# Kernel tuning notes

Hardware: AMD Instinct MI355X
Metric: run time of the kernel (lower is better)

## Reference

```python
import jax, jax.numpy as jnp
import numpy as np

SR = 44100
LOWEST_HZ = 55.0
N_FRAMES = 100
L_ORDER = 5                       # l_filter_order
NC = L_ORDER + 1                  # num_coefficients
NA = L_ORDER + 2                  # num_active_indexes
V = int(SR // LOWEST_HZ) + NA     # coeff_vector_size = 808
N_SAMPLES = 44100


def _nat_cubic_spline_eval(y, t_out):
    """Natural cubic spline through y (n_knots, d) on uniform knots in [0,1],
    evaluated at t_out (T,). Returns (T, d)."""
    n, d = y.shape
    h = 1.0 / (n - 1)
    # second derivatives M: natural BC -> M[0] = M[n-1] = 0, tridiagonal solve
    rhs = 6.0 * (y[2:] - 2.0 * y[1:-1] + y[:-2]) / h        # (n-2, d)
    T = (jnp.diag(jnp.full((n - 2,), 4.0 * h))
         + jnp.diag(jnp.full((n - 3,), h), 1)
         + jnp.diag(jnp.full((n - 3,), h), -1))
    M_in = jnp.linalg.solve(T, rhs)
    M = jnp.concatenate([jnp.zeros((1, d), y.dtype), M_in, jnp.zeros((1, d), y.dtype)])
    idx = jnp.clip((t_out / h).astype(jnp.int32), 0, n - 2)
    f = (t_out - idx.astype(y.dtype) * h)[:, None]          # fractional offset
    y0, y1 = y[idx], y[idx + 1]
    M0, M1 = M[idx], M[idx + 1]
    bcoef = (y1 - y0) / h - h * (2.0 * M0 + M1) / 6.0
    ccoef = 0.5 * M0
    dcoef = (M1 - M0) / (6.0 * h)
    return y0 + f * (bcoef + f * (ccoef + f * dcoef))


def _sample_wise_lpc(x, a):
    """Time-varying all-pole filter: y[t] = x[t] - sum_i a[t, i] * y[t-1-i].
    x: (T,), a: (T, p) -> y: (T,)."""
    p = a.shape[1]

    def step(hist, inp):
        xt, at = inp
        yt = xt - jnp.dot(at, hist)
        hist = jnp.concatenate([yt[None], hist[:-1]])
        return hist, yt

    _, y = jax.lax.scan(step, jnp.zeros((p,), x.dtype), (x, a))
    return y


def setup_inputs() -> dict:
    key = jax.random.key(0)
    k1, k2, k3, k4 = jax.random.split(key, 4)
    # delay in samples, ~[300, 500] -> f0 in [88, 147] Hz, safely inside V=808
    delay_len_frames = 300.0 + 200.0 * jax.random.uniform(k1, (N_FRAMES,), dtype=jnp.float32)
    raw_gain = jnp.full((1,), 2.5, jnp.float32)             # sigmoid -> ~0.924 loop gain
    # raw coeffs uniform in (-2, 0) like the torch init
    raw_coeff_frames = -2.0 * jax.random.uniform(k2, (N_FRAMES, NC), dtype=jnp.float32)
    excitation = jax.random.normal(k3, (N_SAMPLES,), dtype=jnp.float32)
    exc_coefficients = 0.01 * jax.random.normal(k4, (1, N_SAMPLES, 1), dtype=jnp.float32)
    return {"delay_len_frames": delay_len_frames, "raw_gain": raw_gain,
            "raw_coeff_frames": raw_coeff_frames, "excitation": excitation,
            "exc_coefficients": exc_coefficients, "n_samples": N_SAMPLES}


def reference(delay_len_frames, raw_gain, raw_coeff_frames, excitation,
              exc_coefficients, n_samples):
    # constrained, normalized loop-filter coefficients per frame
    gain = jax.nn.sigmoid(raw_gain)                          # (1,)
    sig = jax.nn.sigmoid(raw_coeff_frames)                   # (F, NC)
    b_frames = sig / jnp.sum(sig, -1, keepdims=True) * gain

    # upsample delay + coeffs jointly with one natural cubic spline
    params = jnp.concatenate([delay_len_frames[:, None], b_frames], axis=1)  # (F, NC+1)
    t_out = jnp.linspace(0.0, 1.0, n_samples)
    up = _nat_cubic_spline_eval(params, t_out)               # (T, NC+1)
    delay, b = up[:, 0], up[:, 1:]

    z = jnp.floor(delay).astype(jnp.int32)                   # integer delay
    alfa = delay - jnp.floor(delay)                          # fractional part

    # scatter-build the per-sample sparse filter rows into dense A (T, V)
    cols = z[:, None] + jnp.arange(NA)[None, :]              # (T, NA)
    first = (-(1.0 - alfa) * b[:, 0])[:, None]
    mid = -(alfa[:, None] * b[:, :-1] + (1.0 - alfa)[:, None] * b[:, 1:])
    last = (-alfa * b[:, -1])[:, None]
    vals = jnp.concatenate([first, mid, last], axis=1)       # (T, NA)
    A = jnp.zeros((n_samples, V), jnp.float32).at[
        jnp.arange(n_samples)[:, None], cols].set(vals)

    # excitation shaping (order-1 time-varying all-pole), then KS string loop
    x = _sample_wise_lpc(excitation, exc_coefficients[0])
    y = _sample_wise_lpc(x, A)
    return y
```

## Files before the change

kernel.cpp:

```cpp
#include <hip/hip_runtime.h>

#define NSMP 44100
#define NKNOT 100
#define NIV  (NKNOT - 1)
#define NCC 6
#define NAA 7
#define RING 1024
#define NTH 320
#define SEG ((NSMP + NTH - 1) / NTH)
#define GW 8
#define NHEAT 256
#define HEAT_SLEEPS 6

__device__ __forceinline__ float sigm(float x) { return 1.0f / (1.0f + expf(-x)); }

__device__ __forceinline__ void lean_barrier() {
    asm volatile("s_waitcnt lgkmcnt(0)" ::: "memory");
    __builtin_amdgcn_s_barrier();
    __builtin_amdgcn_sched_barrier(0);
}

__device__ __forceinline__ void compute_rec(const float4 (*CO)[8], int t, bool a,
                                            float* wr, int* raOut) {
    const float H   = 1.0f / 99.0f;
    const float INV = 1.0f / (float)(NSMP - 1);
    if (!a) {
#pragma unroll
        for (int d = 0; d < NAA; ++d) wr[d] = 0.0f;
        *raOut = 0;
        return;
    }
    float tt = (float)t * INV;
    int idx = (int)(tt * 99.0f); if (idx > NIV - 1) idx = NIV - 1;
    float f = tt - (float)idx * H;
    float r[NAA];
#pragma unroll
    for (int c = 0; c < NAA; ++c) {
        float4 k = CO[idx][c];
        r[c] = k.x + f * (k.y + f * (k.z + f * k.w));
    }
    float fl = floorf(r[0]);
    float alfa = r[0] - fl, om = 1.0f - alfa;
    wr[6] = -om * r[1];
    wr[5] = -(alfa * r[1] + om * r[2]);
    wr[4] = -(alfa * r[2] + om * r[3]);
    wr[3] = -(alfa * r[3] + om * r[4]);
    wr[2] = -(alfa * r[4] + om * r[5]);
    wr[1] = -(alfa * r[5] + om * r[6]);
    wr[0] = -alfa * r[6];
    *raOut = (t - 1 - (int)fl - 6) & (RING - 1);
}

__global__ __launch_bounds__(NTH, 1) void diffks_kernel(
    const float* __restrict__ dlf, const float* __restrict__ rg,
    const float* __restrict__ rcf, const float* __restrict__ exc,
    const float* __restrict__ ecoef, float* __restrict__ out,
    float* __restrict__ ws, int ws_ok)
{
    if (blockIdx.x != 0) {
        float v = 1.0f + 0.125f * (float)(blockIdx.x & 7);
#pragma unroll 1
        for (int k = 0; k < HEAT_SLEEPS; ++k) {
            __builtin_amdgcn_s_sleep(127);
            v = fmaf(v, 1.000001f, 1.0e-6f);
        }
        asm volatile("" :: "v"(v));
        if (ws_ok && threadIdx.x == 0) ws[blockIdx.x] = v;
        return;
    }

    __shared__ float  P[NKNOT][NAA];
    __shared__ float  M[NKNOT][NAA];
    __shared__ float4 CO[NIV][8];
    __shared__ float  ring[2 * RING];
    __shared__ float  CPs[NKNOT - 2];
    __shared__ float  IMs[NKNOT - 2];
    __shared__ float  wpS[NTH / 64], wqS[NTH / 64];
    __shared__ int    s_minz;

    const int tid  = threadIdx.x;
    const int lane = tid & 63;
    const int wav  = tid >> 6;
    const float H   = 1.0f / 99.0f;

    if (tid == 0) s_minz = 0x7fffffff;
    for (int i = tid; i < 2 * RING; i += NTH) ring[i] = 0.0f;

    if (tid < NKNOT) {
        float g = sigm(rg[0]);
        float s[NCC];
        float sum = 0.0f;
#pragma unroll
        for (int j = 0; j < NCC; ++j) { s[j] = sigm(rcf[tid * NCC + j]); sum += s[j]; }
        P[tid][0] = dlf[tid];
#pragma unroll
        for (int j = 0; j < NCC; ++j) P[tid][j + 1] = s[j] / sum * g;
    }
    if (tid < NKNOT - 2) {
        float cp = 0.25f;
        int n = tid; if (n > 10) n = 10;
        for (int k = 0; k < n; ++k) cp = 1.0f / (4.0f - cp);
        CPs[tid] = cp;
    }
    __syncthreads();
    if (tid >= 1 && tid < NKNOT - 2) IMs[tid] = 99.0f / (4.0f - CPs[tid - 1]);
    __syncthreads();

    if (tid < NAA) {
        int c = tid;
        float rhs0  = 6.0f * (P[2][c] - 2.0f * P[1][c] + P[0][c]) * 99.0f;
        float dprev = rhs0 * 24.75f;
        M[1][c] = dprev;
        for (int i = 1; i < NKNOT - 2; ++i) {
            float rhs = 6.0f * (P[i + 2][c] - 2.0f * P[i + 1][c] + P[i][c]) * 99.0f;
            float d   = (rhs - H * dprev) * IMs[i];
            M[i + 1][c] = d;
            dprev = d;
        }
        float nxt = M[NKNOT - 2][c];
        for (int i = NKNOT - 4; i >= 0; --i) {
            float v = M[i + 1][c] - CPs[i] * nxt;
            M[i + 1][c] = v;
            nxt = v;
        }
        M[0][c] = 0.0f;
        M[NKNOT - 1][c] = 0.0f;
    }
    __syncthreads();

    if (tid < NIV) {
        float lb = fminf(P[tid][0], P[tid + 1][0])
                 - (H * H * 0.125f) * fmaxf(fabsf(M[tid][0]), fabsf(M[tid + 1][0]));
        atomicMin(&s_minz, (int)floorf(lb));
    }

    for (int iv = tid; iv < NIV; iv += NTH) {
#pragma unroll
        for (int c = 0; c < NAA; ++c) {
            float y0 = P[iv][c], y1 = P[iv + 1][c];
            float m0 = M[iv][c], m1 = M[iv + 1][c];
            float b  = (y1 - y0) * 99.0f - H * (2.0f * m0 + m1) * (1.0f / 6.0f);
            CO[iv][c] = make_float4(y0, b, 0.5f * m0, (m1 - m0) * (99.0f / 6.0f));
        }
    }
    __syncthreads();

    {
        int start = tid * SEG;
        int end   = min(start + SEG, NSMP);
        float p = 1.0f, q = 0.0f;
#pragma unroll 4
        for (int t = start; t < end; ++t) {
            float a2 = ecoef[t];
            q = fmaf(-a2, q, exc[t]);
            p *= -a2;
        }
#pragma unroll
        for (int d = 1; d < 64; d <<= 1) {
            float pp = __shfl_up(p, d);
            float qq = __shfl_up(q, d);
            if (lane >= d) { q = fmaf(p, qq, q); p *= pp; }
        }
        if (lane == 63) { wpS[wav] = p; wqS[wav] = q; }
        float pe = __shfl_up(p, 1);
        float qe = __shfl_up(q, 1);
        if (lane == 0) { pe = 1.0f; qe = 0.0f; }
        __syncthreads();
        float v = 0.0f;
        for (int w = 0; w < wav; ++w) v = fmaf(wpS[w], v, wqS[w]);
        float y = fmaf(pe, v, qe);
#pragma unroll 4
        for (int t = start; t < end; ++t) {
            y = fmaf(-ecoef[t], y, exc[t]);
            out[t] = y;
        }
    }
    __syncthreads();

    int C = s_minz + 1;
    if (C > NTH) C = NTH;
    if (C < 1)  C = 1;
    const int NW   = (NSMP + C - 1) / C;
    const int NCH  = (NW + GW - 1) / GW;
    const int step = GW * C;

    float wA[GW][NAA];
    int   raA[GW];
    float xsA[GW];
#pragma unroll
    for (int g = 0; g < GW; ++g) {
        int t = g * C + tid;
        bool a = (tid < C) && (t < NSMP);
        compute_rec(CO, t, a, wA[g], &raA[g]);
        xsA[g] = a ? out[t] : 0.0f;
    }

    for (int ch = 0; ch < NCH; ++ch) {
        const int W0 = ch * step;
        const int Wn = W0 + step;
        float nx[GW];
#pragma unroll
        for (int g = 0; g < GW; ++g) {
            int tn = Wn + g * C + tid;
            nx[g] = ((tid < C) && (tn < NSMP)) ? out[tn] : 0.0f;
        }
        float wB[GW][NAA];
        int   raB[GW];
#pragma unroll
        for (int g = 0; g < GW; ++g) {
            int t = W0 + g * C + tid;
            bool a = (tid < C) && (t < NSMP);
            const float* rp = &ring[(unsigned)raA[g]];
            float y0 = rp[0], y1 = rp[1], y2 = rp[2], y3 = rp[3];
            float y4 = rp[4], y5 = rp[5], y6 = rp[6];
            {
                int tn = Wn + g * C + tid;
                bool an = (tid < C) && (tn < NSMP);
                compute_rec(CO, tn, an, wB[g], &raB[g]);
            }
            float s = ((wA[g][0] * y0 + wA[g][1] * y1) + (wA[g][2] * y2 + wA[g][3] * y3))
                    + ((wA[g][4] * y4 + wA[g][5] * y5) + wA[g][6] * y6);
            float acc = xsA[g] - s;
            if (a) {
                int wi = t & (RING - 1);
                ring[wi] = acc;
                ring[wi + RING] = acc;
                out[t] = acc;
            }
            lean_barrier();
        }
#pragma unroll
        for (int g = 0; g < GW; ++g) {
#pragma unroll
            for (int d = 0; d < NAA; ++d) wA[g][d] = wB[g][d];
            raA[g] = raB[g];
            xsA[g] = nx[g];
        }
    }
}

extern "C" void kernel_launch(void* const* d_in, const int* in_sizes, int n_in,
                              void* d_out, int out_size, void* d_ws, size_t ws_size,
                              hipStream_t stream) {
    const float* dlf   = (const float*)d_in[0];
    const float* rg    = (const float*)d_in[1];
    const float* rcf   = (const float*)d_in[2];
    const float* exc   = (const float*)d_in[3];
    const float* ecoef = (const float*)d_in[4];
    float* out = (float*)d_out;
    float* ws  = (float*)d_ws;
    int ws_ok = (d_ws != nullptr && ws_size >= (size_t)(NHEAT + 1) * sizeof(float)) ? 1 : 0;
    hipLaunchKernelGGL(diffks_kernel, dim3(1 + NHEAT), dim3(NTH), 0, stream,
                       dlf, rg, rcf, exc, ecoef, out, ws, ws_ok);
}
```

Measured before the change: 138.5 us.

## Split block into producer and consumer waves with an LDS coefficient queue

Doubles the block to 640 threads. Half the threads act as producers: they evaluate the spline filter coefficients, ring offsets and inputs two windows ahead and write them into a 4-deep shared-memory queue. The other half run the serial recurrence and only read ready coefficients from that queue, which takes the coefficient evaluation off the critical path. It also removes the 256 dummy heater blocks, which may change clock behaviour, and adds a barrier per window with twice as many waves taking part.

```diff
diff --git a/kernel.cpp b/kernel.cpp
--- a/kernel.cpp
+++ b/kernel.cpp
@@ -6,11 +6,10 @@
 #define NCC 6
 #define NAA 7
 #define RING 1024
-#define NTH 320
+#define NTH 640
+#define NCONS 320
 #define SEG ((NSMP + NTH - 1) / NTH)
-#define GW 8
-#define NHEAT 256
-#define HEAT_SLEEPS 6
+#define QD 4
 
 __device__ __forceinline__ float sigm(float x) { return 1.0f / (1.0f + expf(-x)); }
 
@@ -54,21 +53,8 @@
 __global__ __launch_bounds__(NTH, 1) void diffks_kernel(
     const float* __restrict__ dlf, const float* __restrict__ rg,
     const float* __restrict__ rcf, const float* __restrict__ exc,
-    const float* __restrict__ ecoef, float* __restrict__ out,
-    float* __restrict__ ws, int ws_ok)
+    const float* __restrict__ ecoef, float* __restrict__ out)
 {
-    if (blockIdx.x != 0) {
-        float v = 1.0f + 0.125f * (float)(blockIdx.x & 7);
-#pragma unroll 1
-        for (int k = 0; k < HEAT_SLEEPS; ++k) {
-            __builtin_amdgcn_s_sleep(127);
-            v = fmaf(v, 1.000001f, 1.0e-6f);
-        }
-        asm volatile("" :: "v"(v));
-        if (ws_ok && threadIdx.x == 0) ws[blockIdx.x] = v;
-        return;
-    }
-
     __shared__ float  P[NKNOT][NAA];
     __shared__ float  M[NKNOT][NAA];
     __shared__ float4 CO[NIV][8];
@@ -77,11 +63,12 @@
     __shared__ float  IMs[NKNOT - 2];
     __shared__ float  wpS[NTH / 64], wqS[NTH / 64];
     __shared__ int    s_minz;
+    __shared__ float  Qp[9][QD][NCONS];
 
     const int tid  = threadIdx.x;
     const int lane = tid & 63;
     const int wav  = tid >> 6;
-    const float H   = 1.0f / 99.0f;
+    const float H  = 1.0f / 99.0f;
 
     if (tid == 0) s_minz = 0x7fffffff;
     for (int i = tid; i < 2 * RING; i += NTH) ring[i] = 0.0f;
@@ -178,64 +165,79 @@
     __syncthreads();
 
     int C = s_minz + 1;
-    if (C > NTH) C = NTH;
+    if (C > NCONS) C = NCONS;
     if (C < 1)  C = 1;
-    const int NW   = (NSMP + C - 1) / C;
-    const int NCH  = (NW + GW - 1) / GW;
-    const int step = GW * C;
-
-    float wA[GW][NAA];
-    int   raA[GW];
-    float xsA[GW];
-#pragma unroll
-    for (int g = 0; g < GW; ++g) {
-        int t = g * C + tid;
-        bool a = (tid < C) && (t < NSMP);
-        compute_rec(CO, t, a, wA[g], &raA[g]);
-        xsA[g] = a ? out[t] : 0.0f;
-    }
-
-    for (int ch = 0; ch < NCH; ++ch) {
-        const int W0 = ch * step;
-        const int Wn = W0 + step;
-        float nx[GW];
-#pragma unroll
-        for (int g = 0; g < GW; ++g) {
-            int tn = Wn + g * C + tid;
-            nx[g] = ((tid < C) && (tn < NSMP)) ? out[tn] : 0.0f;
-        }
-        float wB[GW][NAA];
-        int   raB[GW];
-#pragma unroll
-        for (int g = 0; g < GW; ++g) {
-            int t = W0 + g * C + tid;
+    const int NW = (NSMP + C - 1) / C;
+    const bool isCons = (tid < NCONS);
+    const int  pid    = tid - NCONS;
+
+    float px = 0.0f;
+    if (!isCons) {
+#pragma unroll
+        for (int w = 0; w < 2; ++w) {
+            int t = w * C + pid;
+            bool a = (pid < C) && (t < NSMP);
+            float x2 = a ? out[t] : 0.0f;
+            float wr[NAA]; int ra;
+            compute_rec(CO, t, a, wr, &ra);
+#pragma unroll
+            for (int p = 0; p < 7; ++p) Qp[p][w][pid] = wr[p];
+            Qp[7][w][pid] = x2;
+            Qp[8][w][pid] = __int_as_float(ra);
+        }
+        int t2 = 2 * C + pid;
+        px = ((pid < C) && (t2 < NSMP)) ? out[t2] : 0.0f;
+    }
+    __syncthreads();
+
+    float rw0=0,rw1=0,rw2=0,rw3=0,rw4=0,rw5=0,rw6=0, rx=0;
+    int rra = 0;
+    if (isCons) {
+        rw0 = Qp[0][0][tid]; rw1 = Qp[1][0][tid]; rw2 = Qp[2][0][tid];
+        rw3 = Qp[3][0][tid]; rw4 = Qp[4][0][tid]; rw5 = Qp[5][0][tid];
+        rw6 = Qp[6][0][tid]; rx  = Qp[7][0][tid];
+        rra = __float_as_int(Qp[8][0][tid]);
+    }
+
+    for (int w = 0; w < NW; ++w) {
+        if (isCons) {
+            int t = w * C + tid;
             bool a = (tid < C) && (t < NSMP);
-            const float* rp = &ring[(unsigned)raA[g]];
+            const float* rp = &ring[(unsigned)rra];
             float y0 = rp[0], y1 = rp[1], y2 = rp[2], y3 = rp[3];
             float y4 = rp[4], y5 = rp[5], y6 = rp[6];
-            {
-                int tn = Wn + g * C + tid;
-                bool an = (tid < C) && (tn < NSMP);
-                compute_rec(CO, tn, an, wB[g], &raB[g]);
-            }
-            float s = ((wA[g][0] * y0 + wA[g][1] * y1) + (wA[g][2] * y2 + wA[g][3] * y3))
-                    + ((wA[g][4] * y4 + wA[g][5] * y5) + wA[g][6] * y6);
-            float acc = xsA[g] - s;
+            int slot1 = (w + 1) & (QD - 1);
+            float nw0 = Qp[0][slot1][tid], nw1 = Qp[1][slot1][tid];
+            float nw2 = Qp[2][slot1][tid], nw3 = Qp[3][slot1][tid];
+            float nw4 = Qp[4][slot1][tid], nw5 = Qp[5][slot1][tid];
+            float nw6 = Qp[6][slot1][tid], nx  = Qp[7][slot1][tid];
+            int   nra = __float_as_int(Qp[8][slot1][tid]);
+            float s = ((rw0 * y0 + rw1 * y1) + (rw2 * y2 + rw3 * y3))
+                    + ((rw4 * y4 + rw5 * y5) + rw6 * y6);
+            float acc = rx - s;
             if (a) {
                 int wi = t & (RING - 1);
                 ring[wi] = acc;
                 ring[wi + RING] = acc;
                 out[t] = acc;
             }
-            lean_barrier();
-        }
-#pragma unroll
-        for (int g = 0; g < GW; ++g) {
-#pragma unroll
-            for (int d = 0; d < NAA; ++d) wA[g][d] = wB[g][d];
-            raA[g] = raB[g];
-            xsA[g] = nx[g];
-        }
+            rw0 = nw0; rw1 = nw1; rw2 = nw2; rw3 = nw3;
+            rw4 = nw4; rw5 = nw5; rw6 = nw6; rx = nx; rra = nra;
+        } else {
+            int wt = w + 2;
+            int t  = wt * C + pid;
+            bool a = (pid < C) && (t < NSMP);
+            float wr[NAA]; int ra;
+            compute_rec(CO, t, a, wr, &ra);
+            int slot2 = wt & (QD - 1);
+#pragma unroll
+            for (int p = 0; p < 7; ++p) Qp[p][slot2][pid] = wr[p];
+            Qp[7][slot2][pid] = a ? px : 0.0f;
+            Qp[8][slot2][pid] = __int_as_float(ra);
+            int tn = (wt + 1) * C + pid;
+            px = ((pid < C) && (tn < NSMP)) ? out[tn] : 0.0f;
+        }
+        lean_barrier();
     }
 }
 
@@ -248,8 +250,6 @@
     const float* exc   = (const float*)d_in[3];
     const float* ecoef = (const float*)d_in[4];
     float* out = (float*)d_out;
-    float* ws  = (float*)d_ws;
-    int ws_ok = (d_ws != nullptr && ws_size >= (size_t)(NHEAT + 1) * sizeof(float)) ? 1 : 0;
-    hipLaunchKernelGGL(diffks_kernel, dim3(1 + NHEAT), dim3(NTH), 0, stream,
-                       dlf, rg, rcf, exc, ecoef, out, ws, ws_ok);
-}
+    hipLaunchKernelGGL(diffks_kernel, dim3(1), dim3(NTH), 0, stream,
+                       dlf, rg, rcf, exc, ecoef, out);
+}
```

Result: slower. 153.8 us (+11.1%).
